# Optimization experiments

Hardware: AMD Instinct MI355X
Metric: run time of the kernel (lower is better)

The kernel has to match this reference:

```python
import jax, jax.numpy as jnp
import numpy as np


def setup_inputs() -> dict:
    key = jax.random.key(0)
    k1, k2, k3 = jax.random.split(key, 3)
    B, gd, gh, gw = 4, 8, 16, 16
    H, W = 1024, 1024
    grid = jax.random.normal(k1, (B, 12, gd, gh, gw), dtype=jnp.float32)
    guide = jax.random.uniform(k2, (B, H, W), dtype=jnp.float32)
    image = jax.random.uniform(k3, (B, 3, H, W), dtype=jnp.float32)
    return {"grid": grid, "guide": guide, "image": image}


def _slice_apply(grid, guide, image):
    # grid: [B, 12, gd, gh, gw]; guide: [B, H, W] in [0,1]; image: [B, 3, H, W]
    B, C, gd, gh, gw = grid.shape
    _, h, w = guide.shape
    dt = grid.dtype
    # continuous grid coordinates (Halide reference convention)
    gx = (jnp.arange(w, dtype=dt) + 0.5) * gw / w          # [w]
    gy = (jnp.arange(h, dtype=dt) + 0.5) * gh / h          # [h]
    gz = guide * gd                                        # [B,h,w]
    fx = jnp.floor(gx - 0.5)
    fy = jnp.floor(gy - 0.5)
    fz = jnp.floor(gz - 0.5)
    bidx = jnp.arange(B)[:, None, None]
    coeffs = jnp.zeros((B, h, w, C), dt)
    # 8-corner trilinear gather with tent weights (clamped borders)
    for dz in (0, 1):
        zf = fz + dz
        wz = jnp.maximum(1.0 - jnp.abs(zf + 0.5 - gz), 0.0)       # [B,h,w]
        iz = jnp.clip(zf, 0, gd - 1).astype(jnp.int32)
        for dy in (0, 1):
            yf = fy + dy
            wy = jnp.maximum(1.0 - jnp.abs(yf + 0.5 - gy), 0.0)   # [h]
            iy = jnp.clip(yf, 0, gh - 1).astype(jnp.int32)
            for dx in (0, 1):
                xf = fx + dx
                wx = jnp.maximum(1.0 - jnp.abs(xf + 0.5 - gx), 0.0)  # [w]
                ix = jnp.clip(xf, 0, gw - 1).astype(jnp.int32)
                # gather -> [B,h,w,C]
                g = grid[bidx, :, iz, iy[None, :, None], ix[None, None, :]]
                wgt = wz * wy[None, :, None] * wx[None, None, :]
                coeffs = coeffs + g * wgt[..., None]
    # per-pixel 3x4 affine transform: out_i = sum_j A_ij * in_j + b_i
    co = coeffs.reshape(B, h, w, 3, 4)
    out = jnp.einsum('bhwij,bjhw->bihw', co[..., :3], image) + co[..., 3].transpose(0, 3, 1, 2)
    return out


def reference(grid, guide, image):
    return _slice_apply(grid, guide, image)
```

## Files before the change

### kernel.cpp

```cpp
#include <hip/hip_runtime.h>

#define IMH 1024
#define IMW 1024
#define GD 8
#define GH 16
#define GW 16
#define NC 12
#define ROWS 4

__global__ __launch_bounds__(256) void bsa_kernel(
    const float* __restrict__ grid,
    const float* __restrict__ guide,
    const float* __restrict__ image,
    float* __restrict__ out)
{
    const int y0  = blockIdx.x * ROWS;
    const int b   = blockIdx.y;
    const int tid = threadIdx.x;

    __shared__ __align__(16) float sG[2][GW][GD][NC];
    float* const sbase_ptr = &sG[0][0][0][0];
    const int SBUF = GW * GD * NC;

    const float* gb = grid + (size_t)b * NC * GD * GH * GW;

    int gsrc[6];
    int soff[6];
    #pragma unroll
    for (int k = 0; k < 6; ++k) {
        const int i = tid + 256 * k;
        const int x = i & (GW - 1);
        const int z = (i >> 4) & (GD - 1);
        const int c = i >> 7;
        gsrc[k] = ((c * GD + z) * GH) * GW + x;
        soff[k] = (x * GD + z) * NC + c;
    }

    int   ix0v[4], ix1v[4];
    float txv[4];
    #pragma unroll
    for (int p = 0; p < 4; ++p) {
        const int   x   = tid + 256 * p;
        const float gx  = (x + 0.5f) * ((float)GW / IMW);
        const float fxf = floorf(gx - 0.5f);
        txv[p]  = gx - 0.5f - fxf;
        const int fx = (int)fxf;
        ix0v[p] = min(GW - 1, max(0, fx));
        ix1v[p] = min(GW - 1, max(0, fx + 1));
    }

    {
        const float gy  = (y0 + 0.5f) * ((float)GH / IMH);
        const float fyf = floorf(gy - 0.5f);
        const float ty  = gy - 0.5f - fyf;
        const int   fy  = (int)fyf;
        const int   iy0 = min(GH - 1, max(0, fy));
        const int   iy1 = min(GH - 1, max(0, fy + 1));
        #pragma unroll
        for (int k = 0; k < 6; ++k) {
            const float v0 = gb[gsrc[k] + iy0 * GW];
            const float v1 = gb[gsrc[k] + iy1 * GW];
            sbase_ptr[soff[k]] = v0 + ty * (v1 - v0);
        }
    }
    __syncthreads();

    const size_t plane = (size_t)IMH * IMW;

    #pragma unroll
    for (int j = 0; j < ROWS; ++j) {
        float nv0[6], nv1[6], nty = 0.0f;
        if (j + 1 < ROWS) {
            const int   yn  = y0 + j + 1;
            const float gy  = (yn + 0.5f) * ((float)GH / IMH);
            const float fyf = floorf(gy - 0.5f);
            nty = gy - 0.5f - fyf;
            const int fy  = (int)fyf;
            const int iy0 = min(GH - 1, max(0, fy));
            const int iy1 = min(GH - 1, max(0, fy + 1));
            #pragma unroll
            for (int k = 0; k < 6; ++k) {
                nv0[k] = gb[gsrc[k] + iy0 * GW];
                nv1[k] = gb[gsrc[k] + iy1 * GW];
            }
        }

        const int y = y0 + j;
        const float* gp = guide + ((size_t)b * IMH + y) * IMW;
        const float* ip = image + ((size_t)b * 3 * IMH + y) * IMW;
        float*       op = out   + ((size_t)b * 3 * IMH + y) * IMW;
        const float* S  = sbase_ptr + (j & 1) * SBUF;

        #pragma unroll
        for (int p = 0; p < 4; ++p) {
            const int x = tid + 256 * p;

            const float gv = gp[x];
            const float rv = ip[x];
            const float g2 = ip[x + plane];
            const float bv = ip[x + 2 * plane];

            const float gz  = gv * (float)GD;
            const float fzf = floorf(gz - 0.5f);
            const float tz  = gz - 0.5f - fzf;
            const int   fzi = (int)fzf;
            const int   iz0 = min(GD - 1, max(0, fzi));
            const int   iz1 = min(GD - 1, max(0, fzi + 1));

            const float tx  = txv[p];
            const float w00 = (1.0f - tz) * (1.0f - tx);
            const float w01 = (1.0f - tz) * tx;
            const float w10 = tz * (1.0f - tx);
            const float w11 = tz * tx;

            const float* p00 = S + (ix0v[p] * GD + iz0) * NC;
            const float* p01 = S + (ix1v[p] * GD + iz0) * NC;
            const float* p10 = S + (ix0v[p] * GD + iz1) * NC;
            const float* p11 = S + (ix1v[p] * GD + iz1) * NC;

            float res[3];
            #pragma unroll
            for (int i = 0; i < 3; ++i) {
                const float4 a = *(const float4*)(p00 + 4 * i);
                const float4 c = *(const float4*)(p01 + 4 * i);
                const float4 d = *(const float4*)(p10 + 4 * i);
                const float4 e = *(const float4*)(p11 + 4 * i);
                const float c0 = w00 * a.x + w01 * c.x + w10 * d.x + w11 * e.x;
                const float c1 = w00 * a.y + w01 * c.y + w10 * d.y + w11 * e.y;
                const float c2 = w00 * a.z + w01 * c.z + w10 * d.z + w11 * e.z;
                const float c3 = w00 * a.w + w01 * c.w + w10 * d.w + w11 * e.w;
                res[i] = c0 * rv + c1 * g2 + c2 * bv + c3;
            }

            op[x]             = res[0];
            op[x + plane]     = res[1];
            op[x + 2 * plane] = res[2];
        }

        if (j + 1 < ROWS) {
            float* D = sbase_ptr + ((j + 1) & 1) * SBUF;
            #pragma unroll
            for (int k = 0; k < 6; ++k)
                D[soff[k]] = nv0[k] + nty * (nv1[k] - nv0[k]);
        }
        __syncthreads();
    }
}

extern "C" void kernel_launch(void* const* d_in, const int* in_sizes, int n_in,
                              void* d_out, int out_size, void* d_ws, size_t ws_size,
                              hipStream_t stream) {
    const float* grid  = (const float*)d_in[0];
    const float* guide = (const float*)d_in[1];
    const float* image = (const float*)d_in[2];
    float* out = (float*)d_out;

    const int B = in_sizes[1] / (IMH * IMW);
    dim3 g(IMH / ROWS, B);
    bsa_kernel<<<g, 256, 0, stream>>>(grid, guide, image, out);
}
```

Before: 119.0 us.

## Store y-interpolated grid slice in fp16 with paired z-neighbour layout and packed-half math

The shared-memory grid slice is now stored as fp16, with each z-bin entry holding both its own and the next z-level's 12 coefficients contiguously. Each pixel then needs two 48-byte LDS reads instead of four 48-byte reads. The trilinear blend runs with packed half2 FMAs, and z-border clamping is folded into the weights. This cuts LDS traffic and ALU work, but lowers the precision of the coefficients, which could exceed the accuracy tolerance.

```diff
diff --git a/kernel.cpp b/kernel.cpp
--- a/kernel.cpp
+++ b/kernel.cpp
@@ -1,4 +1,5 @@
 #include <hip/hip_runtime.h>
+#include <hip/hip_fp16.h>
 
 #define IMH 1024
 #define IMW 1024
@@ -6,6 +7,8 @@
 #define GH 16
 #define GW 16
 #define NC 12
+#define NZB 7
+#define ENT 24
 #define ROWS 4
 
 __global__ __launch_bounds__(256) void bsa_kernel(
@@ -18,35 +21,37 @@
     const int b   = blockIdx.y;
     const int tid = threadIdx.x;
 
-    __shared__ __align__(16) float sG[2][GW][GD][NC];
-    float* const sbase_ptr = &sG[0][0][0][0];
-    const int SBUF = GW * GD * NC;
+    __shared__ __align__(16) __half sH[2][GW][NZB][ENT];
+    __half* const sbase = &sH[0][0][0][0];
+    const int SBUF = GW * NZB * ENT;
 
     const float* gb = grid + (size_t)b * NC * GD * GH * GW;
 
-    int gsrc[6];
-    int soff[6];
+    int gsrc[6], sx[6], sz[6], sc[6];
     #pragma unroll
     for (int k = 0; k < 6; ++k) {
         const int i = tid + 256 * k;
-        const int x = i & (GW - 1);
-        const int z = (i >> 4) & (GD - 1);
-        const int c = i >> 7;
-        gsrc[k] = ((c * GD + z) * GH) * GW + x;
-        soff[k] = (x * GD + z) * NC + c;
+        sx[k] = i & (GW - 1);
+        sz[k] = (i >> 4) & (GD - 1);
+        sc[k] = i >> 7;
+        gsrc[k] = ((sc[k] * GD + sz[k]) * GH) * GW + sx[k];
     }
 
-    int   ix0v[4], ix1v[4];
-    float txv[4];
+    int   xo0[4], xo1[4];
+    float wx0v[4], wx1v[4];
     #pragma unroll
     for (int p = 0; p < 4; ++p) {
         const int   x   = tid + 256 * p;
         const float gx  = (x + 0.5f) * ((float)GW / IMW);
         const float fxf = floorf(gx - 0.5f);
-        txv[p]  = gx - 0.5f - fxf;
-        const int fx = (int)fxf;
-        ix0v[p] = min(GW - 1, max(0, fx));
-        ix1v[p] = min(GW - 1, max(0, fx + 1));
+        const float tx  = gx - 0.5f - fxf;
+        const int   fx  = (int)fxf;
+        const int   ix0 = min(GW - 1, max(0, fx));
+        const int   ix1 = min(GW - 1, max(0, fx + 1));
+        xo0[p] = ix0 * (NZB * ENT);
+        xo1[p] = ix1 * (NZB * ENT);
+        wx0v[p] = 1.0f - tx;
+        wx1v[p] = tx;
     }
 
     {
@@ -60,7 +65,10 @@
         for (int k = 0; k < 6; ++k) {
             const float v0 = gb[gsrc[k] + iy0 * GW];
             const float v1 = gb[gsrc[k] + iy1 * GW];
-            sbase_ptr[soff[k]] = v0 + ty * (v1 - v0);
+            const __half h = __float2half(v0 + ty * (v1 - v0));
+            const int x = sx[k], z = sz[k], c = sc[k];
+            if (z < NZB) sH[0][x][z][c] = h;
+            if (z > 0)   sH[0][x][z - 1][NC + c] = h;
         }
     }
     __syncthreads();
@@ -89,7 +97,7 @@
         const float* gp = guide + ((size_t)b * IMH + y) * IMW;
         const float* ip = image + ((size_t)b * 3 * IMH + y) * IMW;
         float*       op = out   + ((size_t)b * 3 * IMH + y) * IMW;
-        const float* S  = sbase_ptr + (j & 1) * SBUF;
+        const __half* S = sbase + (j & 1) * SBUF;
 
         #pragma unroll
         for (int p = 0; p < 4; ++p) {
@@ -104,32 +112,44 @@
             const float fzf = floorf(gz - 0.5f);
             const float tz  = gz - 0.5f - fzf;
             const int   fzi = (int)fzf;
-            const int   iz0 = min(GD - 1, max(0, fzi));
-            const int   iz1 = min(GD - 1, max(0, fzi + 1));
+            const int   zb  = min(NZB - 1, max(0, fzi));
+            const float az  = (fzi < 0) ? 1.0f : ((fzi > NZB - 1) ? 0.0f : 1.0f - tz);
+            const float bz  = (fzi < 0) ? 0.0f : ((fzi > NZB - 1) ? 1.0f : tz);
 
-            const float tx  = txv[p];
-            const float w00 = (1.0f - tz) * (1.0f - tx);
-            const float w01 = (1.0f - tz) * tx;
-            const float w10 = tz * (1.0f - tx);
-            const float w11 = tz * tx;
+            const __half2 wa0 = __float2half2_rn(az * wx0v[p]);
+            const __half2 wb0 = __float2half2_rn(bz * wx0v[p]);
+            const __half2 wa1 = __float2half2_rn(az * wx1v[p]);
+            const __half2 wb1 = __float2half2_rn(bz * wx1v[p]);
 
-            const float* p00 = S + (ix0v[p] * GD + iz0) * NC;
-            const float* p01 = S + (ix1v[p] * GD + iz0) * NC;
-            const float* p10 = S + (ix0v[p] * GD + iz1) * NC;
-            const float* p11 = S + (ix1v[p] * GD + iz1) * NC;
+            const __half* e0 = S + xo0[p] + zb * ENT;
+            const __half* e1 = S + xo1[p] + zb * ENT;
+
+            __half2 A[12], B[12];
+            *(uint4*)(A + 0) = *(const uint4*)(e0);
+            *(uint4*)(A + 4) = *(const uint4*)(e0 + 8);
+            *(uint4*)(A + 8) = *(const uint4*)(e0 + 16);
+            *(uint4*)(B + 0) = *(const uint4*)(e1);
+            *(uint4*)(B + 4) = *(const uint4*)(e1 + 8);
+            *(uint4*)(B + 8) = *(const uint4*)(e1 + 16);
+
+            __half2 cl[6];
+            #pragma unroll
+            for (int d = 0; d < 6; ++d) {
+                __half2 t = __hmul2(wa0, A[d]);
+                t = __hfma2(wb0, A[d + 6], t);
+                t = __hfma2(wa1, B[d], t);
+                t = __hfma2(wb1, B[d + 6], t);
+                cl[d] = t;
+            }
 
             float res[3];
             #pragma unroll
             for (int i = 0; i < 3; ++i) {
-                const float4 a = *(const float4*)(p00 + 4 * i);
-                const float4 c = *(const float4*)(p01 + 4 * i);
-                const float4 d = *(const float4*)(p10 + 4 * i);
-                const float4 e = *(const float4*)(p11 + 4 * i);
-                const float c0 = w00 * a.x + w01 * c.x + w10 * d.x + w11 * e.x;
-                const float c1 = w00 * a.y + w01 * c.y + w10 * d.y + w11 * e.y;
-                const float c2 = w00 * a.z + w01 * c.z + w10 * d.z + w11 * e.z;
-                const float c3 = w00 * a.w + w01 * c.w + w10 * d.w + w11 * e.w;
-                res[i] = c0 * rv + c1 * g2 + c2 * bv + c3;
+                const float c0 = __low2float(cl[2 * i]);
+                const float c1 = __high2float(cl[2 * i]);
+                const float c2 = __low2float(cl[2 * i + 1]);
+                const float c3 = __high2float(cl[2 * i + 1]);
+                res[i] = fmaf(c0, rv, fmaf(c1, g2, fmaf(c2, bv, c3)));
             }
 
             op[x]             = res[0];
@@ -138,10 +158,14 @@
         }
 
         if (j + 1 < ROWS) {
-            float* D = sbase_ptr + ((j + 1) & 1) * SBUF;
+            __half* D = sbase + ((j + 1) & 1) * SBUF;
             #pragma unroll
-            for (int k = 0; k < 6; ++k)
-                D[soff[k]] = nv0[k] + nty * (nv1[k] - nv0[k]);
+            for (int k = 0; k < 6; ++k) {
+                const __half h = __float2half(nv0[k] + nty * (nv1[k] - nv0[k]));
+                const int x = sx[k], z = sz[k], c = sc[k];
+                if (z < NZB) D[(x * NZB + z) * ENT + c] = h;
+                if (z > 0)   D[(x * NZB + (z - 1)) * ENT + NC + c] = h;
+            }
         }
         __syncthreads();
     }
```

After: 121.1 us. Within noise of the previous version (+1.8%).
